# Kernel optimization log

Hardware: AMD Instinct MI355X
Metric: run time of the kernel (lower is better)

Reference implementation:

```python
import math
import jax, jax.numpy as jnp
import numpy as np

H = 1024      # d_model
NHALF = 32    # N // 2
L_LEN = 4096
DT_MIN, DT_MAX = 1e-3, 1e-1


def setup_inputs() -> dict:
    key = jax.random.key(0)
    k1, k2 = jax.random.split(key)
    # C stored as real view of a complex (H, N/2) tensor -> (H, N/2, 2)
    C_ri = jax.random.normal(k1, (H, NHALF, 2), dtype=jnp.float32)
    # log_dt ~ Uniform(log(dt_min), log(dt_max))
    u = jax.random.uniform(k2, (H,), dtype=jnp.float32)
    log_dt = u * (math.log(DT_MAX) - math.log(DT_MIN)) + math.log(DT_MIN)
    # log_A_real = log(0.5 * ones), A_imag = pi * arange(N/2) broadcast over H
    log_A_real = jnp.full((H, NHALF), math.log(0.5), dtype=jnp.float32)
    A_imag = math.pi * jnp.broadcast_to(jnp.arange(NHALF, dtype=jnp.float32), (H, NHALF))
    A_imag = jnp.asarray(A_imag)
    return {"C_ri": C_ri, "log_dt": log_dt, "log_A_real": log_A_real,
            "A_imag": A_imag, "L": L_LEN}


def reference(C_ri, log_dt, log_A_real, A_imag, L):
    dt = jnp.exp(log_dt)                              # (H,)
    C = C_ri[..., 0] + 1j * C_ri[..., 1]              # (H, n) complex
    A = -jnp.exp(log_A_real) + 1j * A_imag            # (H, n) complex
    dtA = A * dt[:, None]                             # (H, n)
    # Vandermonde: exp(dtA * l) for l in [0, L)  -> (H, n, L) complex
    coeffs = dtA[:, :, None] * jnp.arange(L, dtype=jnp.float32)
    lhs = C * (jnp.exp(dtA) - 1.0) / A                # (H, n)
    K_complex = jnp.einsum('hn,hnl->hl', lhs, jnp.exp(coeffs))
    return 2.0 * K_complex.real                       # (H, L) float32
```

## Files before the change

kernel.cpp:

```cpp
#include <hip/hip_runtime.h>
#include <math.h>

#define HDIM 1024
#define NH 32
#define LLEN 4096
#define NT 256
#define LDK 72

typedef __attribute__((ext_vector_type(8))) short bf16x8;
typedef __attribute__((ext_vector_type(4))) float f32x4;

__device__ __forceinline__ unsigned int fbits(float x) {
    return __builtin_bit_cast(unsigned int, x);
}
__device__ __forceinline__ float bitsf(unsigned int u) {
    return __builtin_bit_cast(float, u);
}

__global__ __launch_bounds__(NT, 4) void s4d_kernel(
    const float* __restrict__ C_ri,
    const float* __restrict__ log_dt,
    const float* __restrict__ log_A_real,
    const float* __restrict__ A_imag,
    float* __restrict__ out)
{
    __shared__ unsigned short sAh[64][LDK], sAl[64][LDK];
    __shared__ unsigned short sBh[64][LDK], sBl[64][LDK];

    const int h = blockIdx.x;
    const int tid = threadIdx.x;
    const int n = tid & 31;
    const int hn = h * NH + n;
    const int r0 = tid >> 5;

    const float dt = expf(log_dt[h]);
    const float Ar = -expf(log_A_real[hn]);
    const float Ai = A_imag[hn];
    const float dtAr = Ar * dt;
    const float dtAi = Ai * dt;

    const float er = expf(dtAr);
    float sn, cs;
    sincosf(dtAi, &sn, &cs);
    const float Er = er * cs - 1.0f;
    const float Ei = er * sn;
    const float cr = C_ri[2 * hn + 0];
    const float ci = C_ri[2 * hn + 1];
    const float nr = cr * Er - ci * Ei;
    const float ni = cr * Ei + ci * Er;
    const float inv = 1.0f / (Ar * Ar + Ai * Ai);
    const float lr = (nr * Ar + ni * Ai) * inv;
    const float li = (ni * Ar - nr * Ai) * inv;

    const float re2 = dtAr * 1.4426950408889634f;
    const double sd = (double)dtAi * 0.15915494309189535;
    const double fdd = sd - floor(sd);
    const float phi = (float)(floor(fdd * 4096.0 + 0.5) * (1.0 / 4096.0));
    const float plo = (float)(fdd - (double)phi);

#pragma unroll
    for (int k = 0; k < 8; ++k) {
        const int row = r0 + 8 * k;
        const float m = (float)row;
        const float x = phi * m;
        const float fr = x - floorf(x);
        float rev = fmaf(plo, m, fr);
        rev -= floorf(rev);
        const float ev = exp2f(re2 * m);
        const float zr = ev * __builtin_amdgcn_cosf(rev);
        const float zi = ev * __builtin_amdgcn_sinf(rev);

        const unsigned int ur = fbits(zr), ui = fbits(zi);
        const unsigned int hp = (ur >> 16) | (ui & 0xFFFF0000u);
        const float rl = zr - bitsf(ur & 0xFFFF0000u);
        const float il = zi - bitsf(ui & 0xFFFF0000u);
        const unsigned int lp = (fbits(rl) >> 16) | (fbits(il) & 0xFFFF0000u);
        *(unsigned int*)&sAh[row][2 * n] = hp;
        *(unsigned int*)&sAl[row][2 * n] = lp;
    }

#pragma unroll
    for (int k = 0; k < 8; ++k) {
        const int row = r0 + 8 * k;
        const float m = (float)(row * 64);
        const float x = phi * m;
        const float fr = x - floorf(x);
        float rev = fmaf(plo, m, fr);
        rev -= floorf(rev);
        const float ev = exp2f(re2 * m);
        const float zr = ev * __builtin_amdgcn_cosf(rev);
        const float zi = ev * __builtin_amdgcn_sinf(rev);

        const float br = 2.0f * (lr * zr - li * zi);
        const float bi = -2.0f * (lr * zi + li * zr);

        const unsigned int ur = fbits(br), ui = fbits(bi);
        const unsigned int hp = (ur >> 16) | (ui & 0xFFFF0000u);
        const float rl = br - bitsf(ur & 0xFFFF0000u);
        const float il = bi - bitsf(ui & 0xFFFF0000u);
        const unsigned int lp = (fbits(rl) >> 16) | (fbits(il) & 0xFFFF0000u);
        *(unsigned int*)&sBh[row][2 * n] = hp;
        *(unsigned int*)&sBl[row][2 * n] = lp;
    }
    __syncthreads();

    const int wv = tid >> 6;
    const int lane = tid & 63;
    const int li16 = lane & 15;
    const int lg = lane >> 4;

    f32x4 acc[4];
#pragma unroll
    for (int tc = 0; tc < 4; ++tc) acc[tc] = (f32x4){0.f, 0.f, 0.f, 0.f};

#pragma unroll
    for (int s = 0; s < 6; ++s) {
        const unsigned short (*Am)[LDK] = (s >= 4) ? sAl : sAh;
        const unsigned short (*Bm)[LDK] = (s == 2 || s == 3) ? sBl : sBh;
        const int ko = (s & 1) * 32 + 8 * lg;

        const bf16x8 af = *(const bf16x8*)&Am[16 * wv + li16][ko];
#pragma unroll
        for (int tc = 0; tc < 4; ++tc) {
            const bf16x8 bfr = *(const bf16x8*)&Bm[16 * tc + li16][ko];
            acc[tc] = __builtin_amdgcn_mfma_f32_16x16x32_bf16(af, bfr, acc[tc], 0, 0, 0);
        }
    }

    const int base = h * LLEN + 64 * li16 + 16 * wv + 4 * lg;
#pragma unroll
    for (int tc = 0; tc < 4; ++tc) {
        *(float4*)&out[base + 1024 * tc] =
            make_float4(acc[tc][0], acc[tc][1], acc[tc][2], acc[tc][3]);
    }
}

extern "C" void kernel_launch(void* const* d_in, const int* in_sizes, int n_in,
                              void* d_out, int out_size, void* d_ws, size_t ws_size,
                              hipStream_t stream) {
    const float* C_ri       = (const float*)d_in[0];
    const float* log_dt     = (const float*)d_in[1];
    const float* log_A_real = (const float*)d_in[2];
    const float* A_imag     = (const float*)d_in[3];
    float* out = (float*)d_out;

    s4d_kernel<<<dim3(HDIM), dim3(NT), 0, stream>>>(C_ri, log_dt, log_A_real, A_imag, out);
}
```

Before: 13.28 us.

## Double block threads, use complex recurrence for powers, split MFMA tiles across waves

```diff
diff --git a/kernel.cpp b/kernel.cpp
--- a/kernel.cpp
+++ b/kernel.cpp
@@ -4,18 +4,14 @@
 #define HDIM 1024
 #define NH 32
 #define LLEN 4096
-#define NT 256
+#define NT 512
 #define LDK 72
 
 typedef __attribute__((ext_vector_type(8))) short bf16x8;
 typedef __attribute__((ext_vector_type(4))) float f32x4;
 
-__device__ __forceinline__ unsigned int fbits(float x) {
-    return __builtin_bit_cast(unsigned int, x);
-}
-__device__ __forceinline__ float bitsf(unsigned int u) {
-    return __builtin_bit_cast(float, u);
-}
+__device__ __forceinline__ unsigned int fbits(float x) { return __builtin_bit_cast(unsigned int, x); }
+__device__ __forceinline__ float bitsf(unsigned int u) { return __builtin_bit_cast(float, u); }
 
 __global__ __launch_bounds__(NT, 4) void s4d_kernel(
     const float* __restrict__ C_ri,
@@ -33,15 +29,24 @@
     const int hn = h * NH + n;
     const int r0 = tid >> 5;
 
-    const float dt = expf(log_dt[h]);
-    const float Ar = -expf(log_A_real[hn]);
+    const float LOG2E = 1.4426950408889634f;
+
+    const float dt = exp2f(log_dt[h] * LOG2E);
+    const float Ar = -exp2f(log_A_real[hn] * LOG2E);
     const float Ai = A_imag[hn];
     const float dtAr = Ar * dt;
     const float dtAi = Ai * dt;
+    const float re2 = dtAr * LOG2E;
 
-    const float er = expf(dtAr);
-    float sn, cs;
-    sincosf(dtAi, &sn, &cs);
+    const double sd = (double)dtAi * 0.15915494309189535;
+    const double fdd = sd - floor(sd);
+    const float phi = (float)(floor(fdd * 4096.0 + 0.5) * (1.0 / 4096.0));
+    const float plo = (float)(fdd - (double)phi);
+
+    const float er = exp2f(re2);
+    const float rv = (float)fdd;
+    const float cs = __builtin_amdgcn_cosf(rv);
+    const float sn = __builtin_amdgcn_sinf(rv);
     const float Er = er * cs - 1.0f;
     const float Ei = er * sn;
     const float cr = C_ri[2 * hn + 0];
@@ -52,55 +57,60 @@
     const float lr = (nr * Ar + ni * Ai) * inv;
     const float li = (ni * Ar - nr * Ai) * inv;
 
-    const float re2 = dtAr * 1.4426950408889634f;
-    const double sd = (double)dtAi * 0.15915494309189535;
-    const double fdd = sd - floor(sd);
-    const float phi = (float)(floor(fdd * 4096.0 + 0.5) * (1.0 / 4096.0));
-    const float plo = (float)(fdd - (double)phi);
-
-#pragma unroll
-    for (int k = 0; k < 8; ++k) {
-        const int row = r0 + 8 * k;
-        const float m = (float)row;
+    auto zpow = [&](float m, float& zr, float& zi) {
         const float x = phi * m;
         const float fr = x - floorf(x);
         float rev = fmaf(plo, m, fr);
         rev -= floorf(rev);
         const float ev = exp2f(re2 * m);
-        const float zr = ev * __builtin_amdgcn_cosf(rev);
-        const float zi = ev * __builtin_amdgcn_sinf(rev);
+        zr = ev * __builtin_amdgcn_cosf(rev);
+        zi = ev * __builtin_amdgcn_sinf(rev);
+    };
 
-        const unsigned int ur = fbits(zr), ui = fbits(zi);
-        const unsigned int hp = (ur >> 16) | (ui & 0xFFFF0000u);
-        const float rl = zr - bitsf(ur & 0xFFFF0000u);
-        const float il = zi - bitsf(ui & 0xFFFF0000u);
-        const unsigned int lp = (fbits(rl) >> 16) | (fbits(il) & 0xFFFF0000u);
-        *(unsigned int*)&sAh[row][2 * n] = hp;
-        *(unsigned int*)&sAl[row][2 * n] = lp;
+    {
+        float zr, zi, sr, si;
+        zpow((float)r0, zr, zi);
+        zpow(16.0f, sr, si);
+        int row = r0;
+#pragma unroll
+        for (int k = 0; k < 4; ++k) {
+            const unsigned int urb = fbits(zr), uib = fbits(zi);
+            const unsigned int hp = (urb >> 16) | (uib & 0xFFFF0000u);
+            const float rl = zr - bitsf(urb & 0xFFFF0000u);
+            const float il = zi - bitsf(uib & 0xFFFF0000u);
+            const unsigned int lp = (fbits(rl) >> 16) | (fbits(il) & 0xFFFF0000u);
+            *(unsigned int*)&sAh[row][2 * n] = hp;
+            *(unsigned int*)&sAl[row][2 * n] = lp;
+            const float t = zr * sr - zi * si;
+            zi = zr * si + zi * sr;
+            zr = t;
+            row += 16;
+        }
     }
 
+    {
+        float zr, zi, sr, si;
+        zpow((float)(64 * r0), zr, zi);
+        zpow(1024.0f, sr, si);
+        float ur = lr * zr - li * zi;
+        float ui = lr * zi + li * zr;
+        int row = r0;
 #pragma unroll
-    for (int k = 0; k < 8; ++k) {
-        const int row = r0 + 8 * k;
-        const float m = (float)(row * 64);
-        const float x = phi * m;
-        const float fr = x - floorf(x);
-        float rev = fmaf(plo, m, fr);
-        rev -= floorf(rev);
-        const float ev = exp2f(re2 * m);
-        const float zr = ev * __builtin_amdgcn_cosf(rev);
-        const float zi = ev * __builtin_amdgcn_sinf(rev);
-
-        const float br = 2.0f * (lr * zr - li * zi);
-        const float bi = -2.0f * (lr * zi + li * zr);
-
-        const unsigned int ur = fbits(br), ui = fbits(bi);
-        const unsigned int hp = (ur >> 16) | (ui & 0xFFFF0000u);
-        const float rl = br - bitsf(ur & 0xFFFF0000u);
-        const float il = bi - bitsf(ui & 0xFFFF0000u);
-        const unsigned int lp = (fbits(rl) >> 16) | (fbits(il) & 0xFFFF0000u);
-        *(unsigned int*)&sBh[row][2 * n] = hp;
-        *(unsigned int*)&sBl[row][2 * n] = lp;
+        for (int k = 0; k < 4; ++k) {
+            const float br = ur + ur;
+            const float bi = -(ui + ui);
+            const unsigned int urb = fbits(br), uib = fbits(bi);
+            const unsigned int hp = (urb >> 16) | (uib & 0xFFFF0000u);
+            const float rl = br - bitsf(urb & 0xFFFF0000u);
+            const float il = bi - bitsf(uib & 0xFFFF0000u);
+            const unsigned int lp = (fbits(rl) >> 16) | (fbits(il) & 0xFFFF0000u);
+            *(unsigned int*)&sBh[row][2 * n] = hp;
+            *(unsigned int*)&sBl[row][2 * n] = lp;
+            const float t = ur * sr - ui * si;
+            ui = ur * si + ui * sr;
+            ur = t;
+            row += 16;
+        }
     }
     __syncthreads();
 
@@ -108,30 +118,31 @@
     const int lane = tid & 63;
     const int li16 = lane & 15;
     const int lg = lane >> 4;
+    const int arow = wv & 3;
+    const int tc0 = (wv >> 2) * 2;
 
-    f32x4 acc[4];
-#pragma unroll
-    for (int tc = 0; tc < 4; ++tc) acc[tc] = (f32x4){0.f, 0.f, 0.f, 0.f};
+    f32x4 acc[2];
+    acc[0] = (f32x4){0.f, 0.f, 0.f, 0.f};
+    acc[1] = (f32x4){0.f, 0.f, 0.f, 0.f};
 
 #pragma unroll
     for (int s = 0; s < 6; ++s) {
         const unsigned short (*Am)[LDK] = (s >= 4) ? sAl : sAh;
         const unsigned short (*Bm)[LDK] = (s == 2 || s == 3) ? sBl : sBh;
         const int ko = (s & 1) * 32 + 8 * lg;
-
-        const bf16x8 af = *(const bf16x8*)&Am[16 * wv + li16][ko];
+        const bf16x8 af = *(const bf16x8*)&Am[16 * arow + li16][ko];
 #pragma unroll
-        for (int tc = 0; tc < 4; ++tc) {
-            const bf16x8 bfr = *(const bf16x8*)&Bm[16 * tc + li16][ko];
-            acc[tc] = __builtin_amdgcn_mfma_f32_16x16x32_bf16(af, bfr, acc[tc], 0, 0, 0);
+        for (int t = 0; t < 2; ++t) {
+            const bf16x8 bfr = *(const bf16x8*)&Bm[16 * (tc0 + t) + li16][ko];
+            acc[t] = __builtin_amdgcn_mfma_f32_16x16x32_bf16(af, bfr, acc[t], 0, 0, 0);
         }
     }
 
-    const int base = h * LLEN + 64 * li16 + 16 * wv + 4 * lg;
+    const int rr = 16 * arow + 4 * lg;
 #pragma unroll
-    for (int tc = 0; tc < 4; ++tc) {
-        *(float4*)&out[base + 1024 * tc] =
-            make_float4(acc[tc][0], acc[tc][1], acc[tc][2], acc[tc][3]);
+    for (int t = 0; t < 2; ++t) {
+        const int q = 16 * (tc0 + t) + li16;
+        *(f32x4*)&out[h * LLEN + 64 * q + rr] = acc[t];
     }
 }
 
```

Result: faster. 12.66 us (-4.7%).
